# Optimization experiments

Hardware: AMD Instinct MI355X
Metric: run time of the kernel (lower is better)

The kernel has to match this reference:

```python
import jax, jax.numpy as jnp
import numpy as np

D_INNER = 32
D_STATE = 16
DT_RANK = 32
K = 2


def _cubic_matrix(out_size, in_size):
    # PyTorch bicubic, align_corners=True, a=-0.75, border replicate via index clamp
    a = -0.75
    src = jnp.arange(out_size, dtype=jnp.float32) * (float(in_size - 1) / float(out_size - 1))
    i0 = jnp.floor(src).astype(jnp.int32)
    idx = i0[:, None] + jnp.arange(-1, 3, dtype=jnp.int32)[None, :]  # [out,4]
    d = jnp.abs(src[:, None] - idx.astype(jnp.float32))
    w = jnp.where(d <= 1.0, (a + 2.0) * d**3 - (a + 3.0) * d**2 + 1.0,
                  jnp.where(d < 2.0, a * d**3 - 5.0 * a * d**2 + 8.0 * a * d - 4.0 * a, 0.0))
    idxc = jnp.clip(idx, 0, in_size - 1)
    M = jnp.zeros((out_size, in_size), jnp.float32)
    M = M.at[jnp.arange(out_size)[:, None], idxc].add(w)
    return M


def _upsample_bicubic(x, H, W):
    _, _, h, w = x.shape
    Mh = _cubic_matrix(H, h)
    Mw = _cubic_matrix(W, w)
    return jnp.einsum('Hh,bchw,Ww->bcHW', Mh, x, Mw)


def _conv3x3(x, w, b):
    y = jax.lax.conv_general_dilated(x, w, (1, 1), ((1, 1), (1, 1)),
                                     dimension_numbers=('NCHW', 'OIHW', 'NCHW'))
    return y + b[None, :, None, None]


def _layernorm2d(x, g, b, eps=1e-5):
    # LayerNorm over the channel dim of NCHW
    mu = jnp.mean(x, axis=1, keepdims=True)
    var = jnp.var(x, axis=1, keepdims=True)
    return (x - mu) / jnp.sqrt(var + eps) * g[None, :, None, None] + b[None, :, None, None]


def _selective_scan(u, delta, A, Bs, Cs, Ds, delta_bias):
    # u, delta: [B,K,D,L]; A: [K,D,N]; Bs, Cs: [B,K,N,L]; Ds, delta_bias: [K,D]
    delta = jax.nn.softplus(delta + delta_bias[None, :, :, None])
    Bsz, k, d, L = u.shape
    N = A.shape[-1]

    def step(h, inp):
        u_l, d_l, B_l, C_l = inp  # [B,K,D],[B,K,D],[B,K,N],[B,K,N]
        dA = jnp.exp(d_l[..., None] * A)                     # [B,K,D,N]
        h = dA * h + (d_l * u_l)[..., None] * B_l[:, :, None, :]
        y = jnp.einsum('bkdn,bkn->bkd', h, C_l)
        return h, y

    seq = (jnp.moveaxis(u, -1, 0), jnp.moveaxis(delta, -1, 0),
           jnp.moveaxis(Bs, -1, 0), jnp.moveaxis(Cs, -1, 0))
    h0 = jnp.zeros((Bsz, k, d, N), u.dtype)
    _, ys = jax.lax.scan(step, h0, seq)
    ys = jnp.moveaxis(ys, 0, -1)                              # [B,K,D,L]
    return ys + Ds[None, :, :, None] * u


def _forward(out0, out1, out2, out3, conv0_w, conv0_b, conv1_w, conv1_b,
             conv2_w, conv2_b, conv3_w, conv3_b, x_proj_weight,
             dt_projs_weight, dt_projs_bias, A_logs, Ds, ln_g, ln_b):
    outs = [out0, out1, out2, out3]
    fusion = _conv3x3(out3, conv0_w, conv0_b)                 # [B,32,16,16]
    A = -jnp.exp(A_logs).reshape(K, D_INNER, D_STATE)
    Dsr = Ds.reshape(K, D_INNER)
    convs = [(conv1_w, conv1_b), (conv2_w, conv2_b), (conv3_w, conv3_b)]
    for i in range(3):
        feat = outs[2 - i]
        Bsz, _, H, W = feat.shape
        x = _upsample_bicubic(fusion, H, W)
        x = jnp.concatenate([x, feat], axis=1)
        x = _conv3x3(x, *convs[i])                            # [B,32,H,W]
        L = H * W
        x0 = x.reshape(Bsz, D_INNER, L)                       # row-major scan
        x1 = jnp.swapaxes(x, 2, 3).reshape(Bsz, D_INNER, L)   # column-major scan
        xs = jnp.stack([x0, x1], axis=1)                      # [B,2,32,L]
        x_dbl = jnp.einsum('bkdl,kcd->bkcl', xs, x_proj_weight)
        dts, Bm, Cm = jnp.split(x_dbl, [DT_RANK, DT_RANK + D_STATE], axis=2)
        dts = jnp.einsum('bkrl,kdr->bkdl', dts, dt_projs_weight)
        ys = _selective_scan(xs, dts, A, Bm, Cm, Dsr, dt_projs_bias)
        y1 = jnp.swapaxes(ys[:, 1].reshape(Bsz, D_INNER, W, H), 2, 3).reshape(Bsz, D_INNER, L)
        fusion = (ys[:, 0] + y1).reshape(Bsz, D_INNER, H, W)
        fusion = _layernorm2d(fusion, ln_g, ln_b)
    return fusion


def setup_inputs() -> dict:
    key = jax.random.key(0)
    ks = jax.random.split(key, 12)
    f = lambda k, shape, s: jax.random.normal(k, shape, jnp.float32) * s
    return {
        'out0': jax.random.normal(ks[0], (2, 96, 128, 128), jnp.float32),
        'out1': jax.random.normal(ks[1], (2, 192, 64, 64), jnp.float32),
        'out2': jax.random.normal(ks[2], (2, 384, 32, 32), jnp.float32),
        'out3': jax.random.normal(ks[3], (2, 768, 16, 16), jnp.float32),
        'conv0_w': f(ks[4], (32, 768, 3, 3), 0.02), 'conv0_b': jnp.zeros(32, jnp.float32),
        'conv1_w': f(ks[5], (32, 416, 3, 3), 0.02), 'conv1_b': jnp.zeros(32, jnp.float32),
        'conv2_w': f(ks[6], (32, 224, 3, 3), 0.02), 'conv2_b': jnp.zeros(32, jnp.float32),
        'conv3_w': f(ks[7], (32, 128, 3, 3), 0.02), 'conv3_b': jnp.zeros(32, jnp.float32),
        'x_proj_weight': f(ks[8], (K, DT_RANK + 2 * D_STATE, D_INNER), 0.1),
        'dt_projs_weight': f(ks[9], (K, D_INNER, DT_RANK), 0.1),
        'dt_projs_bias': f(ks[10], (K, D_INNER), 0.5),
        'A_logs': jnp.tile(jnp.log(jnp.arange(1, D_STATE + 1, dtype=jnp.float32))[None, :],
                           (K * D_INNER, 1)),
        'Ds': jnp.ones(K * D_INNER, jnp.float32),
        'ln_g': jnp.ones(32, jnp.float32), 'ln_b': jnp.zeros(32, jnp.float32),
    }


def reference(out0, out1, out2, out3, conv0_w, conv0_b, conv1_w, conv1_b,
              conv2_w, conv2_b, conv3_w, conv3_b, x_proj_weight,
              dt_projs_weight, dt_projs_bias, A_logs, Ds, ln_g, ln_b):
    return _forward(out0, out1, out2, out3, conv0_w, conv0_b, conv1_w, conv1_b,
                    conv2_w, conv2_b, conv3_w, conv3_b, x_proj_weight,
                    dt_projs_weight, dt_projs_bias, A_logs, Ds, ln_g, ln_b)
```

## Files before the change

kernel.cpp:

```cpp
#include <hip/hip_runtime.h>
#include <hip/hip_bf16.h>
#include <math.h>

#define D_INNER 32
#define D_STATE 16
#define KDIRS 2
#define BATCH 2
#define CL 32

__device__ __forceinline__ float cubic_w(float d) {
    const float a = -0.75f;
    float d2 = d * d, d3 = d2 * d;
    if (d <= 1.0f) return (a + 2.0f) * d3 - (a + 3.0f) * d2 + 1.0f;
    if (d < 2.0f)  return a * d3 - 5.0f * a * d2 + 8.0f * a * d - 4.0f * a;
    return 0.0f;
}

__global__ void upsample_kernel(const float* __restrict__ in, float* __restrict__ out,
                                int h, int w, int H, int W, int total) {
    int i = blockIdx.x * 256 + threadIdx.x;
    if (i >= total) return;
    int ox = i % W; int t = i / W; int oy = t % H; int p = t / H;
    const float* ip = in + (size_t)p * h * w;
    float sy = (float)oy * ((float)(h - 1) / (float)(H - 1));
    float sx = (float)ox * ((float)(w - 1) / (float)(W - 1));
    int iy0 = (int)floorf(sy), ix0 = (int)floorf(sx);
    float wy[4], wx[4]; int yi[4], xi[4];
#pragma unroll
    for (int j = 0; j < 4; ++j) {
        int idy = iy0 + j - 1;
        wy[j] = cubic_w(fabsf(sy - (float)idy));
        yi[j] = min(max(idy, 0), h - 1);
        int idx = ix0 + j - 1;
        wx[j] = cubic_w(fabsf(sx - (float)idx));
        xi[j] = min(max(idx, 0), w - 1);
    }
    float acc = 0.f;
#pragma unroll
    for (int jy = 0; jy < 4; ++jy) {
        float rowv = 0.f;
#pragma unroll
        for (int jx = 0; jx < 4; ++jx)
            rowv += wx[jx] * ip[yi[jy] * w + xi[jx]];
        acc += wy[jy] * rowv;
    }
    out[(size_t)p * H * W + (size_t)oy * W + ox] = acc;
}

__global__ void wtrans_all_kernel(const float* __restrict__ w0, const float* __restrict__ w1,
                                  const float* __restrict__ w2, const float* __restrict__ w3,
                                  float* __restrict__ wT) {
    int i = blockIdx.x * 256 + threadIdx.x;
    if (i >= 442368) return;
    const float* src; int Cin, j;
    if (i < 221184)      { src = w0; Cin = 768; j = i; }
    else if (i < 340992) { src = w1; Cin = 416; j = i - 221184; }
    else if (i < 405504) { src = w2; Cin = 224; j = i - 340992; }
    else                 { src = w3; Cin = 128; j = i - 405504; }
    int oc = j & 31;
    int t = (j >> 5) % 9;
    int ic = j / 288;
    wT[i] = src[((size_t)oc * Cin + ic) * 9 + t];
}

__global__ void conv_stage_kernel(const float* __restrict__ up, const float* __restrict__ feat,
                                  int cFeat, const float* __restrict__ wT,
                                  float* __restrict__ partial,
                                  int H, int W, int tilesX, int ICS, int tiles) {
    int b = blockIdx.z, s = blockIdx.y;
    int och = blockIdx.x / tiles;
    int tile = blockIdx.x - och * tiles;
    int tY0 = (tile / tilesX) * 16, tX0 = (tile % tilesX) * 32;
    int tid = threadIdx.x;
    int row = tid >> 4, cx = tid & 15;
    __shared__ float tileS[4][18][35];
    __shared__ float wsh[4][9][16];
    float acc[32];
#pragma unroll
    for (int i = 0; i < 32; ++i) acc[i] = 0.f;
    int icg0 = s * ICS;
    size_t HW = (size_t)H * W;
    for (int icb = 0; icb < ICS; icb += 4) {
        for (int idx = tid; idx < 4 * 612; idx += 256) {
            int ict = idx / 612, rem = idx - ict * 612;
            int r = rem / 34, c = rem - r * 34;
            int icg = icg0 + icb + ict;
            const float* src = (icg < 32)
                ? up + ((size_t)b * 32 + icg) * HW
                : feat + ((size_t)b * cFeat + (icg - 32)) * HW;
            int gy = tY0 + r - 1, gx = tX0 + c - 1;
            tileS[ict][r][c] = (gy >= 0 && gy < H && gx >= 0 && gx < W)
                               ? src[(size_t)gy * W + gx] : 0.f;
        }
        for (int idx = tid; idx < 576; idx += 256) {
            int ict = idx / 144, rem = idx - ict * 144;
            int t = rem >> 4, j = rem & 15;
            wsh[ict][t][j] = wT[(size_t)(icg0 + icb + ict) * 288 + t * 32 + och * 16 + j];
        }
        __syncthreads();
#pragma unroll
        for (int ic4 = 0; ic4 < 4; ++ic4) {
            float tv[3][4];
#pragma unroll
            for (int dy = 0; dy < 3; ++dy)
#pragma unroll
                for (int dx = 0; dx < 4; ++dx)
                    tv[dy][dx] = tileS[ic4][row + dy][2 * cx + dx];
#pragma unroll
            for (int t = 0; t < 9; ++t) {
                int ty = t / 3, tx = t % 3;
                float p0 = tv[ty][tx + 0], p1 = tv[ty][tx + 1];
#pragma unroll
                for (int ocg = 0; ocg < 4; ++ocg) {
                    float4 wv = *(const float4*)&wsh[ic4][t][ocg * 4];
                    acc[(ocg * 4 + 0) * 2 + 0] = fmaf(p0, wv.x, acc[(ocg * 4 + 0) * 2 + 0]);
                    acc[(ocg * 4 + 0) * 2 + 1] = fmaf(p1, wv.x, acc[(ocg * 4 + 0) * 2 + 1]);
                    acc[(ocg * 4 + 1) * 2 + 0] = fmaf(p0, wv.y, acc[(ocg * 4 + 1) * 2 + 0]);
                    acc[(ocg * 4 + 1) * 2 + 1] = fmaf(p1, wv.y, acc[(ocg * 4 + 1) * 2 + 1]);
                    acc[(ocg * 4 + 2) * 2 + 0] = fmaf(p0, wv.z, acc[(ocg * 4 + 2) * 2 + 0]);
                    acc[(ocg * 4 + 2) * 2 + 1] = fmaf(p1, wv.z, acc[(ocg * 4 + 2) * 2 + 1]);
                    acc[(ocg * 4 + 3) * 2 + 0] = fmaf(p0, wv.w, acc[(ocg * 4 + 3) * 2 + 0]);
                    acc[(ocg * 4 + 3) * 2 + 1] = fmaf(p1, wv.w, acc[(ocg * 4 + 3) * 2 + 1]);
                }
            }
        }
        __syncthreads();
    }
    int oy = tY0 + row, ox = tX0 + 2 * cx;
    float* pp = partial + ((size_t)(s * BATCH + b) * 32 + och * 16) * HW + (size_t)oy * W + ox;
#pragma unroll
    for (int oc = 0; oc < 16; ++oc)
        *(float2*)(pp + (size_t)oc * HW) = make_float2(acc[oc * 2], acc[oc * 2 + 1]);
}

__global__ void conv_fus_kernel(const float* __restrict__ feat, int cFeat,
                                const float* __restrict__ wT,
                                float* __restrict__ partial, int ICS) {
    int b = blockIdx.z, s = blockIdx.y;
    int och = blockIdx.x;
    int tid = threadIdx.x;
    int row = tid >> 4, col = tid & 15;
    __shared__ float tileS[4][18][19];
    __shared__ float wsh[4][9][16];
    float acc[16];
#pragma unroll
    for (int i = 0; i < 16; ++i) acc[i] = 0.f;
    int icg0 = s * ICS;
    const int H = 16, W = 16;
    size_t HW = 256;
    for (int icb = 0; icb < ICS; icb += 4) {
        for (int idx = tid; idx < 4 * 324; idx += 256) {
            int ict = idx / 324, rem = idx - ict * 324;
            int r = rem / 18, c = rem - r * 18;
            int icg = icg0 + icb + ict;
            const float* src = feat + ((size_t)b * cFeat + icg) * HW;
            int gy = r - 1, gx = c - 1;
            tileS[ict][r][c] = (gy >= 0 && gy < H && gx >= 0 && gx < W)
                               ? src[(size_t)gy * W + gx] : 0.f;
        }
        for (int idx = tid; idx < 576; idx += 256) {
            int ict = idx / 144, rem = idx - ict * 144;
            int t = rem >> 4, j = rem & 15;
            wsh[ict][t][j] = wT[(size_t)(icg0 + icb + ict) * 288 + t * 32 + och * 16 + j];
        }
        __syncthreads();
#pragma unroll
        for (int ic4 = 0; ic4 < 4; ++ic4) {
            float tv[3][3];
#pragma unroll
            for (int dy = 0; dy < 3; ++dy)
#pragma unroll
                for (int dx = 0; dx < 3; ++dx)
                    tv[dy][dx] = tileS[ic4][row + dy][col + dx];
#pragma unroll
            for (int t = 0; t < 9; ++t) {
                float pv = tv[t / 3][t % 3];
#pragma unroll
                for (int ocg = 0; ocg < 4; ++ocg) {
                    float4 wv = *(const float4*)&wsh[ic4][t][ocg * 4];
                    acc[ocg * 4 + 0] = fmaf(pv, wv.x, acc[ocg * 4 + 0]);
                    acc[ocg * 4 + 1] = fmaf(pv, wv.y, acc[ocg * 4 + 1]);
                    acc[ocg * 4 + 2] = fmaf(pv, wv.z, acc[ocg * 4 + 2]);
                    acc[ocg * 4 + 3] = fmaf(pv, wv.w, acc[ocg * 4 + 3]);
                }
            }
        }
        __syncthreads();
    }
    float* pp = partial + ((size_t)(s * BATCH + b) * 32 + och * 16) * HW + (size_t)row * W + col;
#pragma unroll
    for (int oc = 0; oc < 16; ++oc)
        pp[(size_t)oc * HW] = acc[oc];
}

__global__ void conv_reduce_kernel(const float* __restrict__ partial, const float* __restrict__ bias,
                                   float* __restrict__ out, int S, size_t planeTotal, int HW) {
    size_t i = (size_t)blockIdx.x * 256 + threadIdx.x;
    float s = bias[(i / (size_t)HW) & 31];
    for (int ss = 0; ss < S; ++ss) s += partial[(size_t)ss * planeTotal + i];
    out[i] = s;
}

__global__ void __launch_bounds__(1024) reduce_transpose_kernel(
        const float* __restrict__ partial, const float* __restrict__ bias,
        float* __restrict__ xbuf, float* __restrict__ xT,
        int S, int H, int W, int tilesX) {
    __shared__ float t[32][33];
    int p = blockIdx.y;
    int tile = blockIdx.x;
    int tx = tile % tilesX, ty = tile / tilesX;
    int tid = threadIdx.x;
    int c = tid & 31, r = tid >> 5;
    size_t HW = (size_t)H * W;
    size_t planeTotal = (size_t)BATCH * 32 * HW;
    size_t off = (size_t)p * HW + (size_t)(ty * 32 + r) * W + tx * 32 + c;
    float s = bias[p & 31];
    for (int ss = 0; ss < S; ++ss) s += partial[(size_t)ss * planeTotal + off];
    t[r][c] = s;
    xbuf[off] = s;
    __syncthreads();
    xT[(size_t)p * HW + (size_t)(tx * 32 + r) * H + ty * 32 + c] = t[c][r];
}

__global__ void __launch_bounds__(256) proj_kernel(
        const float* __restrict__ x, const float* __restrict__ xT,
        const float* __restrict__ xpw, const float* __restrict__ dtw,
        const float* __restrict__ dtb,
        float* __restrict__ delta, float* __restrict__ Bm, float* __restrict__ Cm,
        int L) {
    int k = blockIdx.y, b = blockIdx.z;
    int l0 = blockIdx.x * 64;
    int tid = threadIdx.x;
    int li = tid & 63, cg = tid >> 6;
    __shared__ float xsA[32 * 66];
    __shared__ float dtsS[32 * 66];
    __shared__ float wxpS[2048];
    __shared__ float wdtS[1024];
    __shared__ float bdtS[32];
    for (int idx = tid; idx < 2048; idx += 256) wxpS[idx] = xpw[k * 2048 + idx];
    for (int idx = tid; idx < 1024; idx += 256) wdtS[idx] = dtw[k * 1024 + idx];
    if (tid < 32) bdtS[tid] = dtb[k * 32 + tid];
    const float* u = (k == 0 ? x : xT) + (size_t)b * D_INNER * L + l0;
    for (int idx = tid; idx < 2048; idx += 256) {
        int d = idx >> 6, l = idx & 63;
        xsA[d * 66 + l] = u[(size_t)d * L + l];
    }
    __syncthreads();
    float xr[32];
#pragma unroll
    for (int d = 0; d < 32; ++d) xr[d] = xsA[d * 66 + li];
#pragma unroll
    for (int j = 0; j < 8; ++j) {
        int c = cg * 8 + j;
        float s = 0.f;
#pragma unroll
        for (int d4 = 0; d4 < 8; ++d4) {
            float4 wv = *(const float4*)&wxpS[c * 32 + d4 * 4];
            s = fmaf(wv.x, xr[d4 * 4 + 0], s);
            s = fmaf(wv.y, xr[d4 * 4 + 1], s);
            s = fmaf(wv.z, xr[d4 * 4 + 2], s);
            s = fmaf(wv.w, xr[d4 * 4 + 3], s);
        }
        dtsS[c * 66 + li] = s;
    }
    __syncthreads();
    {
        float bv[4], cvv[4];
#pragma unroll
        for (int j = 0; j < 4; ++j) {
            int nB = 32 + cg * 4 + j, nC = 48 + cg * 4 + j;
            float sB = 0.f, sC = 0.f;
#pragma unroll
            for (int d4 = 0; d4 < 8; ++d4) {
                float4 wB = *(const float4*)&wxpS[nB * 32 + d4 * 4];
                float4 wC = *(const float4*)&wxpS[nC * 32 + d4 * 4];
                sB = fmaf(wB.x, xr[d4 * 4 + 0], sB); sC = fmaf(wC.x, xr[d4 * 4 + 0], sC);
                sB = fmaf(wB.y, xr[d4 * 4 + 1], sB); sC = fmaf(wC.y, xr[d4 * 4 + 1], sC);
                sB = fmaf(wB.z, xr[d4 * 4 + 2], sB); sC = fmaf(wC.z, xr[d4 * 4 + 2], sC);
                sB = fmaf(wB.w, xr[d4 * 4 + 3], sB); sC = fmaf(wC.w, xr[d4 * 4 + 3], sC);
            }
            bv[j] = sB; cvv[j] = sC;
        }
        size_t base16 = ((size_t)(b * KDIRS + k) * L + l0 + li) * 16 + cg * 4;
        *(float4*)(Bm + base16) = make_float4(bv[0], bv[1], bv[2], bv[3]);
        *(float4*)(Cm + base16) = make_float4(cvv[0], cvv[1], cvv[2], cvv[3]);
    }
    float dr[32];
#pragma unroll
    for (int r = 0; r < 32; ++r) dr[r] = dtsS[r * 66 + li];
    size_t dbase = (((size_t)b * KDIRS + k) * D_INNER) * L + l0 + li;
#pragma unroll
    for (int j = 0; j < 8; ++j) {
        int dd = cg * 8 + j;
        float s = bdtS[dd];
#pragma unroll
        for (int r4 = 0; r4 < 8; ++r4) {
            float4 wv = *(const float4*)&wdtS[dd * 32 + r4 * 4];
            s = fmaf(wv.x, dr[r4 * 4 + 0], s);
            s = fmaf(wv.y, dr[r4 * 4 + 1], s);
            s = fmaf(wv.z, dr[r4 * 4 + 2], s);
            s = fmaf(wv.w, dr[r4 * 4 + 3], s);
        }
        float sp = (s > 0.f) ? (s + log1pf(expf(-s))) : log1pf(expf(s));
        delta[dbase + (size_t)dd * L] = sp;
    }
}

__global__ void __launch_bounds__(256) scan_pass1(
        const float* __restrict__ x, const float* __restrict__ xT,
        const float* __restrict__ delta, const float* __restrict__ Bm,
        const float* __restrict__ A_logs,
        float* __restrict__ Ac, float* __restrict__ Sc, int L, int C, int CLOG) {
    int idx = blockIdx.x * 256 + threadIdx.x;
    int c = idx & (C - 1);
    int gd = idx >> CLOG;
    int d = gd & 31, bk = gd >> 5;
    int b = gd >> 6;
    int l0 = c * CL;
    const float* uptr = ((bk & 1) == 0 ? x : xT) + ((size_t)b * D_INNER + d) * L + l0;
    const float* dp = delta + (size_t)gd * L + l0;
    const float4* Bp4 = (const float4*)(Bm + ((size_t)bk * L + l0) * 16);
    const float* Ap = A_logs + (size_t)(gd & 63) * 16;
    float Av[16], h[16];
#pragma unroll
    for (int n = 0; n < 16; ++n) { Av[n] = -__expf(Ap[n]); h[n] = 0.f; }
    float sumdl = 0.f;
    for (int j = 0; j < CL; j += 4) {
        float4 dv = *(const float4*)(dp + j);
        float4 uv = *(const float4*)(uptr + j);
#pragma unroll
        for (int e = 0; e < 4; ++e) {
            float dl = e == 0 ? dv.x : e == 1 ? dv.y : e == 2 ? dv.z : dv.w;
            float ul = e == 0 ? uv.x : e == 1 ? uv.y : e == 2 ? uv.z : uv.w;
            float du = dl * ul;
            sumdl += dl;
            const float4* Bp = Bp4 + (size_t)(j + e) * 4;
            float4 B0 = Bp[0], B1 = Bp[1], B2 = Bp[2], B3 = Bp[3];
#define STEP1(nn, bb) { float a = __expf(dl * Av[nn]); h[nn] = fmaf(a, h[nn], du * (bb)); }
            STEP1(0, B0.x) STEP1(1, B0.y) STEP1(2, B0.z) STEP1(3, B0.w)
            STEP1(4, B1.x) STEP1(5, B1.y) STEP1(6, B1.z) STEP1(7, B1.w)
            STEP1(8, B2.x) STEP1(9, B2.y) STEP1(10, B2.z) STEP1(11, B2.w)
            STEP1(12, B3.x) STEP1(13, B3.y) STEP1(14, B3.z) STEP1(15, B3.w)
#undef STEP1
        }
    }
#pragma unroll
    for (int n = 0; n < 16; ++n) {
        size_t o = (size_t)(gd * 16 + n) * C + c;
        Ac[o] = __expf(Av[n] * sumdl);
        Sc[o] = h[n];
    }
}

__global__ void __launch_bounds__(256) scan_stitch(
        const float* __restrict__ Ac, const float* __restrict__ Sc,
        float* __restrict__ Hs, int C) {
    int t = blockIdx.x * 256 + threadIdx.x;
    const float4* Ap = (const float4*)(Ac + (size_t)t * C);
    const float4* Sp = (const float4*)(Sc + (size_t)t * C);
    int gd = t >> 4, n = t & 15;
    float* Ho = Hs + (size_t)gd * C * 16 + n;
    float h = 0.f;
    for (int c4 = 0; c4 < (C >> 2); ++c4) {
        float4 a = Ap[c4], s = Sp[c4];
        Ho[(size_t)(c4 * 4 + 0) * 16] = h; h = fmaf(a.x, h, s.x);
        Ho[(size_t)(c4 * 4 + 1) * 16] = h; h = fmaf(a.y, h, s.y);
        Ho[(size_t)(c4 * 4 + 2) * 16] = h; h = fmaf(a.z, h, s.z);
        Ho[(size_t)(c4 * 4 + 3) * 16] = h; h = fmaf(a.w, h, s.w);
    }
}

__global__ void __launch_bounds__(256) scan_pass2(
        const float* __restrict__ x, const float* __restrict__ xT,
        const float* __restrict__ delta, const float* __restrict__ Bm,
        const float* __restrict__ Cm,
        const float* __restrict__ A_logs, const float* __restrict__ Ds,
        const float* __restrict__ Hs,
        float* __restrict__ ys, int L, int C, int CLOG, int W, int hsh) {
    int idx = blockIdx.x * 256 + threadIdx.x;
    int c = idx & (C - 1);
    int gd = idx >> CLOG;
    int d = gd & 31, bk = gd >> 5;
    int k = bk & 1, b = gd >> 6;
    int l0 = c * CL;
    const float* uptr = (k == 0 ? x : xT) + ((size_t)b * D_INNER + d) * L + l0;
    const float* dp = delta + (size_t)gd * L + l0;
    const float4* Bp4 = (const float4*)(Bm + ((size_t)bk * L + l0) * 16);
    const float4* Cp4 = (const float4*)(Cm + ((size_t)bk * L + l0) * 16);
    const float* Ap = A_logs + (size_t)(gd & 63) * 16;
    float Av[16], h[16];
#pragma unroll
    for (int n = 0; n < 16; ++n) Av[n] = -__expf(Ap[n]);
    const float4* Hp = (const float4*)(Hs + ((size_t)gd * C + c) * 16);
    float4 h0 = Hp[0], h1 = Hp[1], h2 = Hp[2], h3 = Hp[3];
    h[0] = h0.x; h[1] = h0.y; h[2] = h0.z; h[3] = h0.w;
    h[4] = h1.x; h[5] = h1.y; h[6] = h1.z; h[7] = h1.w;
    h[8] = h2.x; h[9] = h2.y; h[10] = h2.z; h[11] = h2.w;
    h[12] = h3.x; h[13] = h3.y; h[14] = h3.z; h[15] = h3.w;
    float Dval = Ds[gd & 63];
    float* yout = ys + (size_t)gd * L;
    int Hm1 = (1 << hsh) - 1;
    for (int j = 0; j < CL; j += 4) {
        float4 dv = *(const float4*)(dp + j);
        float4 uv = *(const float4*)(uptr + j);
        float yb[4];
#pragma unroll
        for (int e = 0; e < 4; ++e) {
            float dl = e == 0 ? dv.x : e == 1 ? dv.y : e == 2 ? dv.z : dv.w;
            float ul = e == 0 ? uv.x : e == 1 ? uv.y : e == 2 ? uv.z : uv.w;
            float du = dl * ul;
            const float4* Bp = Bp4 + (size_t)(j + e) * 4;
            const float4* Cp = Cp4 + (size_t)(j + e) * 4;
            float4 B0 = Bp[0], B1 = Bp[1], B2 = Bp[2], B3 = Bp[3];
            float4 C0 = Cp[0], C1 = Cp[1], C2 = Cp[2], C3 = Cp[3];
            float y = 0.f;
#define STEP(nn, bb, cc) { float a = __expf(dl * Av[nn]); h[nn] = fmaf(a, h[nn], du * (bb)); y = fmaf(h[nn], (cc), y); }
            STEP(0, B0.x, C0.x) STEP(1, B0.y, C0.y) STEP(2, B0.z, C0.z) STEP(3, B0.w, C0.w)
            STEP(4, B1.x, C1.x) STEP(5, B1.y, C1.y) STEP(6, B1.z, C1.z) STEP(7, B1.w, C1.w)
            STEP(8, B2.x, C2.x) STEP(9, B2.y, C2.y) STEP(10, B2.z, C2.z) STEP(11, B2.w, C2.w)
            STEP(12, B3.x, C3.x) STEP(13, B3.y, C3.y) STEP(14, B3.z, C3.z) STEP(15, B3.w, C3.w)
#undef STEP
            y = fmaf(Dval, ul, y);
            if (k == 0) {
                yb[e] = y;
            } else {
                int l = l0 + j + e;
                yout[(l & Hm1) * W + (l >> hsh)] = y;
            }
        }
        if (k == 0)
            *(float4*)(yout + l0 + j) = make_float4(yb[0], yb[1], yb[2], yb[3]);
    }
}

__global__ void combine_ln_kernel(const float* __restrict__ ys, const float* __restrict__ g,
                                  const float* __restrict__ beta, float* __restrict__ outp, int L) {
    int b = blockIdx.y;
    int l = blockIdx.x * 256 + threadIdx.x;
    const float* y0 = ys + ((size_t)b * KDIRS + 0) * D_INNER * L + l;
    const float* y1 = ys + ((size_t)b * KDIRS + 1) * D_INNER * L + l;
    float v[32]; float sum = 0.f;
#pragma unroll
    for (int d = 0; d < 32; ++d) {
        float t = y0[(size_t)d * L] + y1[(size_t)d * L];
        v[d] = t; sum += t;
    }
    float mu = sum * (1.0f / 32.0f);
    float var = 0.f;
#pragma unroll
    for (int d = 0; d < 32; ++d) { float t = v[d] - mu; var += t * t; }
    var *= (1.0f / 32.0f);
    float inv = 1.0f / sqrtf(var + 1e-5f);
#pragma unroll
    for (int d = 0; d < 32; ++d)
        outp[((size_t)b * D_INNER + d) * L + l] = (v[d] - mu) * inv * g[d] + beta[d];
}

extern "C" void kernel_launch(void* const* d_in, const int* in_sizes, int n_in,
                              void* d_out, int out_size, void* d_ws, size_t ws_size,
                              hipStream_t stream) {
    const float* out0 = (const float*)d_in[0];
    const float* out1 = (const float*)d_in[1];
    const float* out2 = (const float*)d_in[2];
    const float* out3 = (const float*)d_in[3];
    const float* cw[4] = {(const float*)d_in[4], (const float*)d_in[6],
                          (const float*)d_in[8], (const float*)d_in[10]};
    const float* cb[4] = {(const float*)d_in[5], (const float*)d_in[7],
                          (const float*)d_in[9], (const float*)d_in[11]};
    const float* xpw    = (const float*)d_in[12];
    const float* dtw    = (const float*)d_in[13];
    const float* dtb    = (const float*)d_in[14];
    const float* A_logs = (const float*)d_in[15];
    const float* Ds     = (const float*)d_in[16];
    const float* ln_g   = (const float*)d_in[17];
    const float* ln_b   = (const float*)d_in[18];

    const size_t MF = 1u << 20;
    float* ws    = (float*)d_ws;
    float* fus   = ws;
    float* Hst   = ws + 1 * MF;
    float* up    = ws + 2 * MF;
    float* xbuf  = ws + 3 * MF;
    float* xTbuf = ws + 4 * MF;
    float* delta = ws + 5 * MF;
    float* Bm    = ws + 7 * MF;
    float* Cm    = ws + 8 * MF;
    float* ysbuf = ws + 9 * MF;
    float* Ac    = ws + 11 * MF;
    float* Sc    = ws + 12 * MF;
    float* wT    = ws + 13 * MF;
    float* partial = ws + 14 * MF;

    wtrans_all_kernel<<<(442368 + 255) / 256, 256, 0, stream>>>(cw[0], cw[1], cw[2], cw[3], wT);
    float* wT_f  = wT;
    float* wT_s1 = wT + 221184;
    float* wT_s2 = wT + 340992;
    float* wT_s3 = wT + 405504;

    {
        int Cin = 768, ICS = 8, S = Cin / ICS;
        conv_fus_kernel<<<dim3(2, S, BATCH), 256, 0, stream>>>(out3, Cin, wT_f, partial, ICS);
        size_t planeTotal = (size_t)BATCH * 32 * 256;
        conv_reduce_kernel<<<planeTotal / 256, 256, 0, stream>>>(
            partial, cb[0], fus, S, planeTotal, 256);
    }

    struct Stage { int h, w, H, W, Cf, ICS, hsh; const float* feat; const float* wt; const float* b3; };
    Stage st[3] = {
        {16, 16,  32,  32, 384,  8, 5, out2, wT_s1, cb[1]},
        {32, 32,  64,  64, 192,  8, 6, out1, wT_s2, cb[2]},
        {64, 64, 128, 128,  96, 16, 7, out0, wT_s3, cb[3]},
    };

    for (int i = 0; i < 3; ++i) {
        int H = st[i].H, W = st[i].W;
        int L = H * W;
        int h = st[i].h, w = st[i].w;
        int total = BATCH * 32 * H * W;
        upsample_kernel<<<total / 256, 256, 0, stream>>>(fus, up, h, w, H, W, total);

        int Cin = 32 + st[i].Cf;
        int ICS = st[i].ICS, S = Cin / ICS;
        int tilesX = W / 32, tiles = (H / 16) * tilesX;
        conv_stage_kernel<<<dim3(tiles * 2, S, BATCH), 256, 0, stream>>>(
            up, st[i].feat, st[i].Cf, st[i].wt, partial, H, W, tilesX, ICS, tiles);

        int ttX = W / 32;
        reduce_transpose_kernel<<<dim3((H / 32) * ttX, BATCH * 32), 1024, 0, stream>>>(
            partial, cb[i + 1], xbuf, xTbuf, S, H, W, ttX);

        proj_kernel<<<dim3(L / 64, KDIRS, BATCH), 256, 0, stream>>>(
            xbuf, xTbuf, xpw, dtw, dtb, delta, Bm, Cm, L);

        int C = L / CL;
        int CLOG = (C == 32) ? 5 : (C == 128) ? 7 : 9;
        int passBlocks = (128 * C) / 256;
        scan_pass1<<<passBlocks, 256, 0, stream>>>(xbuf, xTbuf, delta, Bm, A_logs, Ac, Sc, L, C, CLOG);
        scan_stitch<<<8, 256, 0, stream>>>(Ac, Sc, Hst, C);
        scan_pass2<<<passBlocks, 256, 0, stream>>>(xbuf, xTbuf, delta, Bm, Cm, A_logs, Ds, Hst,
                                                   ysbuf, L, C, CLOG, W, st[i].hsh);

        float* dst = (i == 2) ? (float*)d_out : fus;
        combine_ln_kernel<<<dim3(L / 256, BATCH), 256, 0, stream>>>(ysbuf, ln_g, ln_b, dst, L);
    }
}
```

Measured before the change: 604.9 us.

## Fuse SSM stages into cooperative persistent kernel and widen conv blocks

Replaces the five per-stage launches (projection, scan pass1, stitch, pass2, combine+layernorm) with a single cooperative kernel of 256 blocks that runs each phase in a grid-stride loop, separated by grid-wide syncs. A fallback to the separate kernels is kept in case the cooperative launch fails. The 3x3 conv kernel now uses 512-thread blocks that cover both 16-channel output halves, so the input tile is loaded once and shared instead of twice. This cuts launch overhead and duplicated tile loads, but grid syncs and a fixed block count may underuse the GPU on the larger stages.

```diff
diff --git a/kernel.cpp b/kernel.cpp
--- a/kernel.cpp
+++ b/kernel.cpp
@@ -1,6 +1,9 @@
 #include <hip/hip_runtime.h>
 #include <hip/hip_bf16.h>
+#include <hip/hip_cooperative_groups.h>
 #include <math.h>
+
+namespace cg = cooperative_groups;
 
 #define D_INNER 32
 #define D_STATE 16
@@ -63,25 +66,27 @@
     wT[i] = src[((size_t)oc * Cin + ic) * 9 + t];
 }
 
-__global__ void conv_stage_kernel(const float* __restrict__ up, const float* __restrict__ feat,
-                                  int cFeat, const float* __restrict__ wT,
-                                  float* __restrict__ partial,
-                                  int H, int W, int tilesX, int ICS, int tiles) {
+__global__ void __launch_bounds__(512) conv_stage_kernel(
+        const float* __restrict__ up, const float* __restrict__ feat,
+        int cFeat, const float* __restrict__ wT,
+        float* __restrict__ partial,
+        int H, int W, int tilesX, int ICS) {
     int b = blockIdx.z, s = blockIdx.y;
-    int och = blockIdx.x / tiles;
-    int tile = blockIdx.x - och * tiles;
+    int tile = blockIdx.x;
     int tY0 = (tile / tilesX) * 16, tX0 = (tile % tilesX) * 32;
     int tid = threadIdx.x;
-    int row = tid >> 4, cx = tid & 15;
+    int och = tid >> 8;
+    int t256 = tid & 255;
+    int row = t256 >> 4, cx = t256 & 15;
     __shared__ float tileS[4][18][35];
-    __shared__ float wsh[4][9][16];
+    __shared__ float wsh[4][9][32];
     float acc[32];
 #pragma unroll
     for (int i = 0; i < 32; ++i) acc[i] = 0.f;
     int icg0 = s * ICS;
     size_t HW = (size_t)H * W;
     for (int icb = 0; icb < ICS; icb += 4) {
-        for (int idx = tid; idx < 4 * 612; idx += 256) {
+        for (int idx = tid; idx < 4 * 612; idx += 512) {
             int ict = idx / 612, rem = idx - ict * 612;
             int r = rem / 34, c = rem - r * 34;
             int icg = icg0 + icb + ict;
@@ -92,10 +97,10 @@
             tileS[ict][r][c] = (gy >= 0 && gy < H && gx >= 0 && gx < W)
                                ? src[(size_t)gy * W + gx] : 0.f;
         }
-        for (int idx = tid; idx < 576; idx += 256) {
-            int ict = idx / 144, rem = idx - ict * 144;
-            int t = rem >> 4, j = rem & 15;
-            wsh[ict][t][j] = wT[(size_t)(icg0 + icb + ict) * 288 + t * 32 + och * 16 + j];
+        for (int idx = tid; idx < 1152; idx += 512) {
+            int ict = idx / 288, rem = idx - ict * 288;
+            int t = rem >> 5, j = rem & 31;
+            wsh[ict][t][j] = wT[(size_t)(icg0 + icb + ict) * 288 + t * 32 + j];
         }
         __syncthreads();
 #pragma unroll
@@ -112,7 +117,7 @@
                 float p0 = tv[ty][tx + 0], p1 = tv[ty][tx + 1];
 #pragma unroll
                 for (int ocg = 0; ocg < 4; ++ocg) {
-                    float4 wv = *(const float4*)&wsh[ic4][t][ocg * 4];
+                    float4 wv = *(const float4*)&wsh[ic4][t][och * 16 + ocg * 4];
                     acc[(ocg * 4 + 0) * 2 + 0] = fmaf(p0, wv.x, acc[(ocg * 4 + 0) * 2 + 0]);
                     acc[(ocg * 4 + 0) * 2 + 1] = fmaf(p1, wv.x, acc[(ocg * 4 + 0) * 2 + 1]);
                     acc[(ocg * 4 + 1) * 2 + 0] = fmaf(p0, wv.y, acc[(ocg * 4 + 1) * 2 + 0]);
@@ -222,21 +227,15 @@
     xT[(size_t)p * HW + (size_t)(tx * 32 + r) * H + ty * 32 + c] = t[c][r];
 }
 
-__global__ void __launch_bounds__(256) proj_kernel(
+
+__device__ __forceinline__ void proj_body(
+        int k, int b, int l0, int tid,
         const float* __restrict__ x, const float* __restrict__ xT,
         const float* __restrict__ xpw, const float* __restrict__ dtw,
         const float* __restrict__ dtb,
         float* __restrict__ delta, float* __restrict__ Bm, float* __restrict__ Cm,
-        int L) {
-    int k = blockIdx.y, b = blockIdx.z;
-    int l0 = blockIdx.x * 64;
-    int tid = threadIdx.x;
-    int li = tid & 63, cg = tid >> 6;
-    __shared__ float xsA[32 * 66];
-    __shared__ float dtsS[32 * 66];
-    __shared__ float wxpS[2048];
-    __shared__ float wdtS[1024];
-    __shared__ float bdtS[32];
+        int L, float* xsA, float* dtsS, float* wxpS, float* wdtS, float* bdtS) {
+    int li = tid & 63, cgi = tid >> 6;
     for (int idx = tid; idx < 2048; idx += 256) wxpS[idx] = xpw[k * 2048 + idx];
     for (int idx = tid; idx < 1024; idx += 256) wdtS[idx] = dtw[k * 1024 + idx];
     if (tid < 32) bdtS[tid] = dtb[k * 32 + tid];
@@ -251,7 +250,7 @@
     for (int d = 0; d < 32; ++d) xr[d] = xsA[d * 66 + li];
 #pragma unroll
     for (int j = 0; j < 8; ++j) {
-        int c = cg * 8 + j;
+        int c = cgi * 8 + j;
         float s = 0.f;
 #pragma unroll
         for (int d4 = 0; d4 < 8; ++d4) {
@@ -268,7 +267,7 @@
         float bv[4], cvv[4];
 #pragma unroll
         for (int j = 0; j < 4; ++j) {
-            int nB = 32 + cg * 4 + j, nC = 48 + cg * 4 + j;
+            int nB = 32 + cgi * 4 + j, nC = 48 + cgi * 4 + j;
             float sB = 0.f, sC = 0.f;
 #pragma unroll
             for (int d4 = 0; d4 < 8; ++d4) {
@@ -281,7 +280,7 @@
             }
             bv[j] = sB; cvv[j] = sC;
         }
-        size_t base16 = ((size_t)(b * KDIRS + k) * L + l0 + li) * 16 + cg * 4;
+        size_t base16 = ((size_t)(b * KDIRS + k) * L + l0 + li) * 16 + cgi * 4;
         *(float4*)(Bm + base16) = make_float4(bv[0], bv[1], bv[2], bv[3]);
         *(float4*)(Cm + base16) = make_float4(cvv[0], cvv[1], cvv[2], cvv[3]);
     }
@@ -291,7 +290,7 @@
     size_t dbase = (((size_t)b * KDIRS + k) * D_INNER) * L + l0 + li;
 #pragma unroll
     for (int j = 0; j < 8; ++j) {
-        int dd = cg * 8 + j;
+        int dd = cgi * 8 + j;
         float s = bdtS[dd];
 #pragma unroll
         for (int r4 = 0; r4 < 8; ++r4) {
@@ -306,12 +305,11 @@
     }
 }
 
-__global__ void __launch_bounds__(256) scan_pass1(
-        const float* __restrict__ x, const float* __restrict__ xT,
+__device__ __forceinline__ void pass1_body(
+        int idx, const float* __restrict__ x, const float* __restrict__ xT,
         const float* __restrict__ delta, const float* __restrict__ Bm,
         const float* __restrict__ A_logs,
         float* __restrict__ Ac, float* __restrict__ Sc, int L, int C, int CLOG) {
-    int idx = blockIdx.x * 256 + threadIdx.x;
     int c = idx & (C - 1);
     int gd = idx >> CLOG;
     int d = gd & 31, bk = gd >> 5;
@@ -352,10 +350,9 @@
     }
 }
 
-__global__ void __launch_bounds__(256) scan_stitch(
-        const float* __restrict__ Ac, const float* __restrict__ Sc,
+__device__ __forceinline__ void stitch_body(
+        int t, const float* __restrict__ Ac, const float* __restrict__ Sc,
         float* __restrict__ Hs, int C) {
-    int t = blockIdx.x * 256 + threadIdx.x;
     const float4* Ap = (const float4*)(Ac + (size_t)t * C);
     const float4* Sp = (const float4*)(Sc + (size_t)t * C);
     int gd = t >> 4, n = t & 15;
@@ -370,14 +367,13 @@
     }
 }
 
-__global__ void __launch_bounds__(256) scan_pass2(
-        const float* __restrict__ x, const float* __restrict__ xT,
+__device__ __forceinline__ void pass2_body(
+        int idx, const float* __restrict__ x, const float* __restrict__ xT,
         const float* __restrict__ delta, const float* __restrict__ Bm,
         const float* __restrict__ Cm,
         const float* __restrict__ A_logs, const float* __restrict__ Ds,
         const float* __restrict__ Hs,
         float* __restrict__ ys, int L, int C, int CLOG, int W, int hsh) {
-    int idx = blockIdx.x * 256 + threadIdx.x;
     int c = idx & (C - 1);
     int gd = idx >> CLOG;
     int d = gd & 31, bk = gd >> 5;
@@ -433,10 +429,11 @@
     }
 }
 
-__global__ void combine_ln_kernel(const float* __restrict__ ys, const float* __restrict__ g,
-                                  const float* __restrict__ beta, float* __restrict__ outp, int L) {
-    int b = blockIdx.y;
-    int l = blockIdx.x * 256 + threadIdx.x;
+__device__ __forceinline__ void combine_body(
+        int i, const float* __restrict__ ys, const float* __restrict__ g,
+        const float* __restrict__ beta, float* __restrict__ outp, int L) {
+    int b = i / L;
+    int l = i - b * L;
     const float* y0 = ys + ((size_t)b * KDIRS + 0) * D_INNER * L + l;
     const float* y1 = ys + ((size_t)b * KDIRS + 1) * D_INNER * L + l;
     float v[32]; float sum = 0.f;
@@ -454,6 +451,96 @@
 #pragma unroll
     for (int d = 0; d < 32; ++d)
         outp[((size_t)b * D_INNER + d) * L + l] = (v[d] - mu) * inv * g[d] + beta[d];
+}
+
+__global__ void __launch_bounds__(256) ssm_mega_kernel(
+        const float* __restrict__ x, const float* __restrict__ xT,
+        const float* __restrict__ xpw, const float* __restrict__ dtw,
+        const float* __restrict__ dtb,
+        float* __restrict__ delta, float* __restrict__ Bm, float* __restrict__ Cm,
+        const float* __restrict__ A_logs, const float* __restrict__ Ds,
+        float* __restrict__ Ac, float* __restrict__ Sc, float* __restrict__ Hst,
+        float* __restrict__ ys, const float* __restrict__ lng, const float* __restrict__ lnb,
+        float* __restrict__ outp,
+        int L, int C, int CLOG, int W, int hsh) {
+    cg::grid_group gridg = cg::this_grid();
+    int tid = threadIdx.x;
+    int NB = gridDim.x;
+    __shared__ float xsA[32 * 66];
+    __shared__ float dtsS[32 * 66];
+    __shared__ float wxpS[2048];
+    __shared__ float wdtS[1024];
+    __shared__ float bdtS[32];
+
+    int unitsP = C << 1;
+    for (int unit = blockIdx.x; unit < unitsP; unit += NB) {
+        __syncthreads();
+        int lb = unit & ((C >> 1) - 1);
+        int rest = unit >> (CLOG - 1);
+        int k = rest & 1, b = rest >> 1;
+        proj_body(k, b, lb * 64, tid, x, xT, xpw, dtw, dtb, delta, Bm, Cm, L,
+                  xsA, dtsS, wxpS, wdtS, bdtS);
+    }
+    gridg.sync();
+
+    for (int idx = blockIdx.x * 256 + tid; idx < (C << 7); idx += NB * 256)
+        pass1_body(idx, x, xT, delta, Bm, A_logs, Ac, Sc, L, C, CLOG);
+    gridg.sync();
+
+    for (int t = blockIdx.x * 256 + tid; t < 2048; t += NB * 256)
+        stitch_body(t, Ac, Sc, Hst, C);
+    gridg.sync();
+
+    for (int idx = blockIdx.x * 256 + tid; idx < (C << 7); idx += NB * 256)
+        pass2_body(idx, x, xT, delta, Bm, Cm, A_logs, Ds, Hst, ys, L, C, CLOG, W, hsh);
+    gridg.sync();
+
+    for (int i = blockIdx.x * 256 + tid; i < 2 * L; i += NB * 256)
+        combine_body(i, ys, lng, lnb, outp, L);
+}
+
+__global__ void __launch_bounds__(256) proj_kernel(
+        const float* __restrict__ x, const float* __restrict__ xT,
+        const float* __restrict__ xpw, const float* __restrict__ dtw,
+        const float* __restrict__ dtb,
+        float* __restrict__ delta, float* __restrict__ Bm, float* __restrict__ Cm, int L) {
+    __shared__ float xsA[32 * 66];
+    __shared__ float dtsS[32 * 66];
+    __shared__ float wxpS[2048];
+    __shared__ float wdtS[1024];
+    __shared__ float bdtS[32];
+    proj_body(blockIdx.y, blockIdx.z, blockIdx.x * 64, threadIdx.x,
+              x, xT, xpw, dtw, dtb, delta, Bm, Cm, L, xsA, dtsS, wxpS, wdtS, bdtS);
+}
+
+__global__ void __launch_bounds__(256) scan_pass1_k(
+        const float* __restrict__ x, const float* __restrict__ xT,
+        const float* __restrict__ delta, const float* __restrict__ Bm,
+        const float* __restrict__ A_logs,
+        float* __restrict__ Ac, float* __restrict__ Sc, int L, int C, int CLOG) {
+    pass1_body(blockIdx.x * 256 + threadIdx.x, x, xT, delta, Bm, A_logs, Ac, Sc, L, C, CLOG);
+}
+
+__global__ void __launch_bounds__(256) scan_stitch_k(
+        const float* __restrict__ Ac, const float* __restrict__ Sc,
+        float* __restrict__ Hs, int C) {
+    stitch_body(blockIdx.x * 256 + threadIdx.x, Ac, Sc, Hs, C);
+}
+
+__global__ void __launch_bounds__(256) scan_pass2_k(
+        const float* __restrict__ x, const float* __restrict__ xT,
+        const float* __restrict__ delta, const float* __restrict__ Bm,
+        const float* __restrict__ Cm,
+        const float* __restrict__ A_logs, const float* __restrict__ Ds,
+        const float* __restrict__ Hs,
+        float* __restrict__ ys, int L, int C, int CLOG, int W, int hsh) {
+    pass2_body(blockIdx.x * 256 + threadIdx.x, x, xT, delta, Bm, Cm, A_logs, Ds, Hs,
+               ys, L, C, CLOG, W, hsh);
+}
+
+__global__ void combine_ln_kernel(const float* __restrict__ ys, const float* __restrict__ g,
+                                  const float* __restrict__ beta, float* __restrict__ outp, int L) {
+    combine_body(blockIdx.y * L + blockIdx.x * 256 + threadIdx.x, ys, g, beta, outp, L);
 }
 
 extern "C" void kernel_launch(void* const* d_in, const int* in_sizes, int n_in,
@@ -513,34 +600,44 @@
     };
 
     for (int i = 0; i < 3; ++i) {
-        int H = st[i].H, W = st[i].W;
-        int L = H * W;
+        int H = st[i].H, Wv = st[i].W;
+        int L = H * Wv;
         int h = st[i].h, w = st[i].w;
-        int total = BATCH * 32 * H * W;
-        upsample_kernel<<<total / 256, 256, 0, stream>>>(fus, up, h, w, H, W, total);
+        int total = BATCH * 32 * H * Wv;
+        upsample_kernel<<<total / 256, 256, 0, stream>>>(fus, up, h, w, H, Wv, total);
 
         int Cin = 32 + st[i].Cf;
         int ICS = st[i].ICS, S = Cin / ICS;
-        int tilesX = W / 32, tiles = (H / 16) * tilesX;
-        conv_stage_kernel<<<dim3(tiles * 2, S, BATCH), 256, 0, stream>>>(
-            up, st[i].feat, st[i].Cf, st[i].wt, partial, H, W, tilesX, ICS, tiles);
-
-        int ttX = W / 32;
-        reduce_transpose_kernel<<<dim3((H / 32) * ttX, BATCH * 32), 1024, 0, stream>>>(
-            partial, cb[i + 1], xbuf, xTbuf, S, H, W, ttX);
-
-        proj_kernel<<<dim3(L / 64, KDIRS, BATCH), 256, 0, stream>>>(
-            xbuf, xTbuf, xpw, dtw, dtb, delta, Bm, Cm, L);
+        int tilesX = Wv / 32, tiles = (H / 16) * tilesX;
+        conv_stage_kernel<<<dim3(tiles, S, BATCH), 512, 0, stream>>>(
+            up, st[i].feat, st[i].Cf, st[i].wt, partial, H, Wv, tilesX, ICS);
+
+        reduce_transpose_kernel<<<dim3((H / 32) * tilesX, BATCH * 32), 1024, 0, stream>>>(
+            partial, cb[i + 1], xbuf, xTbuf, S, H, Wv, tilesX);
 
         int C = L / CL;
         int CLOG = (C == 32) ? 5 : (C == 128) ? 7 : 9;
-        int passBlocks = (128 * C) / 256;
-        scan_pass1<<<passBlocks, 256, 0, stream>>>(xbuf, xTbuf, delta, Bm, A_logs, Ac, Sc, L, C, CLOG);
-        scan_stitch<<<8, 256, 0, stream>>>(Ac, Sc, Hst, C);
-        scan_pass2<<<passBlocks, 256, 0, stream>>>(xbuf, xTbuf, delta, Bm, Cm, A_logs, Ds, Hst,
-                                                   ysbuf, L, C, CLOG, W, st[i].hsh);
-
+        int hshv = st[i].hsh;
         float* dst = (i == 2) ? (float*)d_out : fus;
-        combine_ln_kernel<<<dim3(L / 256, BATCH), 256, 0, stream>>>(ysbuf, ln_g, ln_b, dst, L);
-    }
-}
+        void* margs[] = {
+            (void*)&xbuf, (void*)&xTbuf, (void*)&xpw, (void*)&dtw, (void*)&dtb,
+            (void*)&delta, (void*)&Bm, (void*)&Cm, (void*)&A_logs, (void*)&Ds,
+            (void*)&Ac, (void*)&Sc, (void*)&Hst, (void*)&ysbuf,
+            (void*)&ln_g, (void*)&ln_b, (void*)&dst,
+            (void*)&L, (void*)&C, (void*)&CLOG, (void*)&Wv, (void*)&hshv
+        };
+        hipError_t err = hipLaunchCooperativeKernel((void*)ssm_mega_kernel,
+                                                    dim3(256), dim3(256), margs, 0, stream);
+        if (err != hipSuccess) {
+            proj_kernel<<<dim3(L / 64, KDIRS, BATCH), 256, 0, stream>>>(
+                xbuf, xTbuf, xpw, dtw, dtb, delta, Bm, Cm, L);
+            int passBlocks = (128 * C) / 256;
+            scan_pass1_k<<<passBlocks, 256, 0, stream>>>(xbuf, xTbuf, delta, Bm, A_logs,
+                                                         Ac, Sc, L, C, CLOG);
+            scan_stitch_k<<<8, 256, 0, stream>>>(Ac, Sc, Hst, C);
+            scan_pass2_k<<<passBlocks, 256, 0, stream>>>(xbuf, xTbuf, delta, Bm, Cm, A_logs,
+                                                         Ds, Hst, ysbuf, L, C, CLOG, Wv, hshv);
+            combine_ln_kernel<<<dim3(L / 256, BATCH), 256, 0, stream>>>(ysbuf, ln_g, ln_b, dst, L);
+        }
+    }
+}
```

After: 976.3 us. 1.61x slower.

## Fuse projection with scan pass1 and merge conv output-channel halves per block

Applied to the files above, without the earlier changes.

The projection kernel now also runs the first chunked-scan pass. It reuses the x, delta and B values it already holds in shared memory, with one thread per (d, n) chain, instead of re-reading them from global memory in a separate kernel. The conv stage kernel now runs 512 threads so both 16-channel output halves share one input tile load, halving tile traffic and block count. The cost is higher register and shared-memory pressure, and less parallelism in the scan inner loop.

```diff
diff --git a/kernel.cpp b/kernel.cpp
--- a/kernel.cpp
+++ b/kernel.cpp
@@ -63,25 +63,27 @@
     wT[i] = src[((size_t)oc * Cin + ic) * 9 + t];
 }
 
-__global__ void conv_stage_kernel(const float* __restrict__ up, const float* __restrict__ feat,
-                                  int cFeat, const float* __restrict__ wT,
-                                  float* __restrict__ partial,
-                                  int H, int W, int tilesX, int ICS, int tiles) {
+__global__ void __launch_bounds__(512) conv_stage_kernel(
+        const float* __restrict__ up, const float* __restrict__ feat,
+        int cFeat, const float* __restrict__ wT,
+        float* __restrict__ partial,
+        int H, int W, int tilesX, int ICS) {
     int b = blockIdx.z, s = blockIdx.y;
-    int och = blockIdx.x / tiles;
-    int tile = blockIdx.x - och * tiles;
+    int tile = blockIdx.x;
     int tY0 = (tile / tilesX) * 16, tX0 = (tile % tilesX) * 32;
     int tid = threadIdx.x;
-    int row = tid >> 4, cx = tid & 15;
+    int och = tid >> 8;
+    int t256 = tid & 255;
+    int row = t256 >> 4, cx = t256 & 15;
     __shared__ float tileS[4][18][35];
-    __shared__ float wsh[4][9][16];
+    __shared__ float wsh[4][9][32];
     float acc[32];
 #pragma unroll
     for (int i = 0; i < 32; ++i) acc[i] = 0.f;
     int icg0 = s * ICS;
     size_t HW = (size_t)H * W;
     for (int icb = 0; icb < ICS; icb += 4) {
-        for (int idx = tid; idx < 4 * 612; idx += 256) {
+        for (int idx = tid; idx < 4 * 612; idx += 512) {
             int ict = idx / 612, rem = idx - ict * 612;
             int r = rem / 34, c = rem - r * 34;
             int icg = icg0 + icb + ict;
@@ -92,10 +94,10 @@
             tileS[ict][r][c] = (gy >= 0 && gy < H && gx >= 0 && gx < W)
                                ? src[(size_t)gy * W + gx] : 0.f;
         }
-        for (int idx = tid; idx < 576; idx += 256) {
-            int ict = idx / 144, rem = idx - ict * 144;
-            int t = rem >> 4, j = rem & 15;
-            wsh[ict][t][j] = wT[(size_t)(icg0 + icb + ict) * 288 + t * 32 + och * 16 + j];
+        for (int idx = tid; idx < 1152; idx += 512) {
+            int ict = idx / 288, rem = idx - ict * 288;
+            int t = rem >> 5, j = rem & 31;
+            wsh[ict][t][j] = wT[(size_t)(icg0 + icb + ict) * 288 + t * 32 + j];
         }
         __syncthreads();
 #pragma unroll
@@ -112,7 +114,7 @@
                 float p0 = tv[ty][tx + 0], p1 = tv[ty][tx + 1];
 #pragma unroll
                 for (int ocg = 0; ocg < 4; ++ocg) {
-                    float4 wv = *(const float4*)&wsh[ic4][t][ocg * 4];
+                    float4 wv = *(const float4*)&wsh[ic4][t][och * 16 + ocg * 4];
                     acc[(ocg * 4 + 0) * 2 + 0] = fmaf(p0, wv.x, acc[(ocg * 4 + 0) * 2 + 0]);
                     acc[(ocg * 4 + 0) * 2 + 1] = fmaf(p1, wv.x, acc[(ocg * 4 + 0) * 2 + 1]);
                     acc[(ocg * 4 + 1) * 2 + 0] = fmaf(p0, wv.y, acc[(ocg * 4 + 1) * 2 + 0]);
@@ -222,18 +224,20 @@
     xT[(size_t)p * HW + (size_t)(tx * 32 + r) * H + ty * 32 + c] = t[c][r];
 }
 
-__global__ void __launch_bounds__(256) proj_kernel(
+__global__ void __launch_bounds__(256) proj_scan1_kernel(
         const float* __restrict__ x, const float* __restrict__ xT,
         const float* __restrict__ xpw, const float* __restrict__ dtw,
-        const float* __restrict__ dtb,
+        const float* __restrict__ dtb, const float* __restrict__ A_logs,
         float* __restrict__ delta, float* __restrict__ Bm, float* __restrict__ Cm,
-        int L) {
+        float* __restrict__ Ac, float* __restrict__ Sc,
+        int L, int C) {
     int k = blockIdx.y, b = blockIdx.z;
     int l0 = blockIdx.x * 64;
     int tid = threadIdx.x;
-    int li = tid & 63, cg = tid >> 6;
+    int li = tid & 63, cgi = tid >> 6;
     __shared__ float xsA[32 * 66];
     __shared__ float dtsS[32 * 66];
+    __shared__ float bS[16 * 66];
     __shared__ float wxpS[2048];
     __shared__ float wdtS[1024];
     __shared__ float bdtS[32];
@@ -251,7 +255,7 @@
     for (int d = 0; d < 32; ++d) xr[d] = xsA[d * 66 + li];
 #pragma unroll
     for (int j = 0; j < 8; ++j) {
-        int c = cg * 8 + j;
+        int c = cgi * 8 + j;
         float s = 0.f;
 #pragma unroll
         for (int d4 = 0; d4 < 8; ++d4) {
@@ -268,7 +272,7 @@
         float bv[4], cvv[4];
 #pragma unroll
         for (int j = 0; j < 4; ++j) {
-            int nB = 32 + cg * 4 + j, nC = 48 + cg * 4 + j;
+            int nB = 32 + cgi * 4 + j, nC = 48 + cgi * 4 + j;
             float sB = 0.f, sC = 0.f;
 #pragma unroll
             for (int d4 = 0; d4 < 8; ++d4) {
@@ -280,18 +284,20 @@
                 sB = fmaf(wB.w, xr[d4 * 4 + 3], sB); sC = fmaf(wC.w, xr[d4 * 4 + 3], sC);
             }
             bv[j] = sB; cvv[j] = sC;
-        }
-        size_t base16 = ((size_t)(b * KDIRS + k) * L + l0 + li) * 16 + cg * 4;
+            bS[(cgi * 4 + j) * 66 + li] = sB;
+        }
+        size_t base16 = ((size_t)(b * KDIRS + k) * L + l0 + li) * 16 + cgi * 4;
         *(float4*)(Bm + base16) = make_float4(bv[0], bv[1], bv[2], bv[3]);
         *(float4*)(Cm + base16) = make_float4(cvv[0], cvv[1], cvv[2], cvv[3]);
     }
     float dr[32];
 #pragma unroll
     for (int r = 0; r < 32; ++r) dr[r] = dtsS[r * 66 + li];
+    __syncthreads();
     size_t dbase = (((size_t)b * KDIRS + k) * D_INNER) * L + l0 + li;
 #pragma unroll
     for (int j = 0; j < 8; ++j) {
-        int dd = cg * 8 + j;
+        int dd = cgi * 8 + j;
         float s = bdtS[dd];
 #pragma unroll
         for (int r4 = 0; r4 < 8; ++r4) {
@@ -303,52 +309,31 @@
         }
         float sp = (s > 0.f) ? (s + log1pf(expf(-s))) : log1pf(expf(s));
         delta[dbase + (size_t)dd * L] = sp;
-    }
-}
-
-__global__ void __launch_bounds__(256) scan_pass1(
-        const float* __restrict__ x, const float* __restrict__ xT,
-        const float* __restrict__ delta, const float* __restrict__ Bm,
-        const float* __restrict__ A_logs,
-        float* __restrict__ Ac, float* __restrict__ Sc, int L, int C, int CLOG) {
-    int idx = blockIdx.x * 256 + threadIdx.x;
-    int c = idx & (C - 1);
-    int gd = idx >> CLOG;
-    int d = gd & 31, bk = gd >> 5;
-    int b = gd >> 6;
-    int l0 = c * CL;
-    const float* uptr = ((bk & 1) == 0 ? x : xT) + ((size_t)b * D_INNER + d) * L + l0;
-    const float* dp = delta + (size_t)gd * L + l0;
-    const float4* Bp4 = (const float4*)(Bm + ((size_t)bk * L + l0) * 16);
-    const float* Ap = A_logs + (size_t)(gd & 63) * 16;
-    float Av[16], h[16];
-#pragma unroll
-    for (int n = 0; n < 16; ++n) { Av[n] = -__expf(Ap[n]); h[n] = 0.f; }
-    float sumdl = 0.f;
-    for (int j = 0; j < CL; j += 4) {
-        float4 dv = *(const float4*)(dp + j);
-        float4 uv = *(const float4*)(uptr + j);
-#pragma unroll
-        for (int e = 0; e < 4; ++e) {
-            float dl = e == 0 ? dv.x : e == 1 ? dv.y : e == 2 ? dv.z : dv.w;
-            float ul = e == 0 ? uv.x : e == 1 ? uv.y : e == 2 ? uv.z : uv.w;
-            float du = dl * ul;
+        dtsS[dd * 66 + li] = sp;
+    }
+    __syncthreads();
+    int gdbase = (b * KDIRS + k) * D_INNER;
+    int c0 = l0 >> 5;
+#pragma unroll
+    for (int iter = 0; iter < 4; ++iter) {
+        int chain = iter * 256 + tid;
+        int cl = chain >> 9;
+        int rem = chain & 511;
+        int d = rem >> 4, n = rem & 15;
+        float Av = -__expf(A_logs[(k * D_INNER + d) * 16 + n]);
+        float h = 0.f, sumdl = 0.f;
+        const float* dS = dtsS + d * 66 + cl * 32;
+        const float* uS = xsA + d * 66 + cl * 32;
+        const float* BS = bS + n * 66 + cl * 32;
+#pragma unroll
+        for (int ll = 0; ll < 32; ++ll) {
+            float dl = dS[ll], ul = uS[ll], Bl = BS[ll];
+            h = fmaf(__expf(dl * Av), h, dl * ul * Bl);
             sumdl += dl;
-            const float4* Bp = Bp4 + (size_t)(j + e) * 4;
-            float4 B0 = Bp[0], B1 = Bp[1], B2 = Bp[2], B3 = Bp[3];
-#define STEP1(nn, bb) { float a = __expf(dl * Av[nn]); h[nn] = fmaf(a, h[nn], du * (bb)); }
-            STEP1(0, B0.x) STEP1(1, B0.y) STEP1(2, B0.z) STEP1(3, B0.w)
-            STEP1(4, B1.x) STEP1(5, B1.y) STEP1(6, B1.z) STEP1(7, B1.w)
-            STEP1(8, B2.x) STEP1(9, B2.y) STEP1(10, B2.z) STEP1(11, B2.w)
-            STEP1(12, B3.x) STEP1(13, B3.y) STEP1(14, B3.z) STEP1(15, B3.w)
-#undef STEP1
-        }
-    }
-#pragma unroll
-    for (int n = 0; n < 16; ++n) {
-        size_t o = (size_t)(gd * 16 + n) * C + c;
-        Ac[o] = __expf(Av[n] * sumdl);
-        Sc[o] = h[n];
+        }
+        size_t o = (size_t)((gdbase + d) * 16 + n) * C + (c0 + cl);
+        Ac[o] = __expf(Av * sumdl);
+        Sc[o] = h;
     }
 }
 
@@ -513,32 +498,29 @@
     };
 
     for (int i = 0; i < 3; ++i) {
-        int H = st[i].H, W = st[i].W;
-        int L = H * W;
+        int H = st[i].H, Wv = st[i].W;
+        int L = H * Wv;
         int h = st[i].h, w = st[i].w;
-        int total = BATCH * 32 * H * W;
-        upsample_kernel<<<total / 256, 256, 0, stream>>>(fus, up, h, w, H, W, total);
+        int total = BATCH * 32 * H * Wv;
+        upsample_kernel<<<total / 256, 256, 0, stream>>>(fus, up, h, w, H, Wv, total);
 
         int Cin = 32 + st[i].Cf;
         int ICS = st[i].ICS, S = Cin / ICS;
-        int tilesX = W / 32, tiles = (H / 16) * tilesX;
-        conv_stage_kernel<<<dim3(tiles * 2, S, BATCH), 256, 0, stream>>>(
-            up, st[i].feat, st[i].Cf, st[i].wt, partial, H, W, tilesX, ICS, tiles);
-
-        int ttX = W / 32;
-        reduce_transpose_kernel<<<dim3((H / 32) * ttX, BATCH * 32), 1024, 0, stream>>>(
-            partial, cb[i + 1], xbuf, xTbuf, S, H, W, ttX);
-
-        proj_kernel<<<dim3(L / 64, KDIRS, BATCH), 256, 0, stream>>>(
-            xbuf, xTbuf, xpw, dtw, dtb, delta, Bm, Cm, L);
+        int tilesX = Wv / 32, tiles = (H / 16) * tilesX;
+        conv_stage_kernel<<<dim3(tiles, S, BATCH), 512, 0, stream>>>(
+            up, st[i].feat, st[i].Cf, st[i].wt, partial, H, Wv, tilesX, ICS);
+
+        reduce_transpose_kernel<<<dim3((H / 32) * tilesX, BATCH * 32), 1024, 0, stream>>>(
+            partial, cb[i + 1], xbuf, xTbuf, S, H, Wv, tilesX);
 
         int C = L / CL;
         int CLOG = (C == 32) ? 5 : (C == 128) ? 7 : 9;
-        int passBlocks = (128 * C) / 256;
-        scan_pass1<<<passBlocks, 256, 0, stream>>>(xbuf, xTbuf, delta, Bm, A_logs, Ac, Sc, L, C, CLOG);
+        proj_scan1_kernel<<<dim3(L / 64, KDIRS, BATCH), 256, 0, stream>>>(
+            xbuf, xTbuf, xpw, dtw, dtb, A_logs, delta, Bm, Cm, Ac, Sc, L, C);
+
         scan_stitch<<<8, 256, 0, stream>>>(Ac, Sc, Hst, C);
-        scan_pass2<<<passBlocks, 256, 0, stream>>>(xbuf, xTbuf, delta, Bm, Cm, A_logs, Ds, Hst,
-                                                   ysbuf, L, C, CLOG, W, st[i].hsh);
+        scan_pass2<<<(128 * C) / 256, 256, 0, stream>>>(
+            xbuf, xTbuf, delta, Bm, Cm, A_logs, Ds, Hst, ysbuf, L, C, CLOG, Wv, st[i].hsh);
 
         float* dst = (i == 2) ? (float*)d_out : fus;
         combine_ln_kernel<<<dim3(L / 256, BATCH), 256, 0, stream>>>(ysbuf, ln_g, ln_b, dst, L);
```

After: 583.0 us. 3.6% less time.
